# Kernel optimization log

Measured on AMD Instinct MI355X. Metric: run time of the kernel, lower is better.

## Reference

```python
import jax, jax.numpy as jnp
import numpy as np

H = 2048          # hidden_size
M = 512           # moe_intermediate_size
E = 8             # n_routed_experts
TOP_K = 2         # num_experts_per_tok
N_SHARED = 2      # n_shared_experts -> shared intermediate = M * N_SHARED
MS = M * N_SHARED
B, S = 2, 1024


def setup_inputs() -> dict:
    key = jax.random.key(0)
    ks = jax.random.split(key, 9)
    sc = 0.02
    return {
        "hidden_states": jax.random.normal(ks[0], (B, S, H), dtype=jnp.float32),
        "gate_w": jax.random.normal(ks[1], (E, H), dtype=jnp.float32) * sc,
        "Wg": jax.random.normal(ks[2], (E, H, M), dtype=jnp.float32) * sc,   # gate_proj per expert
        "Wu": jax.random.normal(ks[3], (E, H, M), dtype=jnp.float32) * sc,   # up_proj per expert
        "Wd": jax.random.normal(ks[4], (E, M, H), dtype=jnp.float32) * sc,   # down_proj per expert
        "sWg": jax.random.normal(ks[5], (H, MS), dtype=jnp.float32) * sc,    # shared gate_proj
        "sWu": jax.random.normal(ks[6], (H, MS), dtype=jnp.float32) * sc,    # shared up_proj
        "sWd": jax.random.normal(ks[7], (MS, H), dtype=jnp.float32) * sc,    # shared down_proj
    }


def reference(hidden_states, gate_w, Wg, Wu, Wd, sWg, sWu, sWd):
    b, s, h = hidden_states.shape
    x = hidden_states.reshape(-1, h)                     # [N, H]
    n = x.shape[0]

    # --- MoEGate: top-k routing with softmax over the selected logits ---
    logits = x @ gate_w.T                                # [N, E]
    topk_vals, topk_idx = jax.lax.top_k(logits, TOP_K)   # [N, K]
    w = jax.nn.softmax(topk_vals, axis=-1)               # softmax scoring over top-k
    # per-token combine weight for every expert (zero where not routed)
    comb = jnp.zeros((n, E), x.dtype).at[jnp.arange(n)[:, None], topk_idx].add(w)

    # --- Routed experts (SwiGLU MLP per expert); combine is the sparse
    #     weight matrix `comb`, mathematically identical to torch dispatch ---
    g = jnp.einsum('nh,ehm->enm', x, Wg)                 # [E, N, M]
    u = jnp.einsum('nh,ehm->enm', x, Wu)
    eo = jnp.einsum('enm,emh->enh', jax.nn.silu(g) * u, Wd)  # [E, N, H]
    y = jnp.einsum('ne,enh->nh', comb, eo)               # weighted combine

    # --- Shared experts (dense SwiGLU MLP on all tokens) ---
    y = y + (jax.nn.silu(x @ sWg) * (x @ sWu)) @ sWd
    return y.reshape(b, s, h)
```

## Files before the change

### kernel.cpp

```cpp
#include <hip/hip_runtime.h>

#define H 2048
#define MDIM 512
#define NE 8
#define MS 1024
#define NTOK 2048
#define ACT_R_ROWS 5120

typedef unsigned short u16;
typedef __attribute__((ext_vector_type(8))) short s16x8;
typedef __attribute__((ext_vector_type(4))) float f32x4;

__device__ inline u16 f2bf(float f) {
  unsigned u = __builtin_bit_cast(unsigned, f);
  u = (u + 0x7fffu + ((u >> 16) & 1u)) >> 16;
  return (u16)u;
}
__device__ inline float bf2f(u16 v) {
  return __builtin_bit_cast(float, (unsigned)v << 16);
}

__device__ inline f32x4 mfma16(s16x8 a, s16x8 b, f32x4 c) {
  return __builtin_amdgcn_mfma_f32_16x16x32_bf16(a, b, c, 0, 0, 0);
}

__device__ inline void gload16(const void* g, void* l) {
  __builtin_amdgcn_global_load_lds(
      (const __attribute__((address_space(1))) unsigned int*)g,
      (__attribute__((address_space(3))) unsigned int*)l, 16, 0, 0);
}


__global__ void k_cvt(const float* __restrict__ src, u16* __restrict__ dst, int n8) {
  int i = blockIdx.x * 256 + threadIdx.x;
  if (i >= n8) return;
  const f32x4* s = (const f32x4*)src;
  f32x4 a = s[2 * i + 0], b = s[2 * i + 1];
  s16x8 o;
  o[0] = (short)f2bf(a[0]); o[1] = (short)f2bf(a[1]);
  o[2] = (short)f2bf(a[2]); o[3] = (short)f2bf(a[3]);
  o[4] = (short)f2bf(b[0]); o[5] = (short)f2bf(b[1]);
  o[6] = (short)f2bf(b[2]); o[7] = (short)f2bf(b[3]);
  ((s16x8*)dst)[i] = o;
}

__device__ inline void tile_t64(const float* __restrict__ src, u16* __restrict__ dst,
                                int R, int C, int bx, int by) {
  __shared__ u16 tt[64][66];
  int c0 = bx * 64, r0 = by * 64;
  int t = threadIdx.x;
  int cq = (t & 15) * 4, rr = t >> 4;
  #pragma unroll
  for (int i = 0; i < 4; i++) {
    int row = rr + i * 16;
    f32x4 v = *(const f32x4*)&src[(long)(r0 + row) * C + c0 + cq];
    tt[cq + 0][row] = f2bf(v[0]);
    tt[cq + 1][row] = f2bf(v[1]);
    tt[cq + 2][row] = f2bf(v[2]);
    tt[cq + 3][row] = f2bf(v[3]);
  }
  __syncthreads();
  int c = t >> 2, ch = t & 3;
  #pragma unroll
  for (int h = 0; h < 2; h++) {
    int chunk = ch + h * 4;
    const u16* p = &tt[c][chunk * 8];
    s16x8 o;
    #pragma unroll
    for (int w0 = 0; w0 < 8; w0++) o[w0] = (short)p[w0];
    *(s16x8*)&dst[(long)(c0 + c) * R + r0 + chunk * 8] = o;
  }
}

__global__ __launch_bounds__(256) void k_prep(
    const float* __restrict__ Wg, const float* __restrict__ Wu,
    const float* __restrict__ Wd, const float* __restrict__ sWg,
    const float* __restrict__ sWu, const float* __restrict__ sWd,
    u16* __restrict__ WgT, u16* __restrict__ WuT, u16* __restrict__ WdT,
    u16* __restrict__ sWgT, u16* __restrict__ sWuT, u16* __restrict__ sWdT) {
  int b = blockIdx.x;
  const float* src; u16* dst; int R, C, lb;
  if (b < 2048) {
    lb = b; R = H; C = MDIM;
    int z = lb >> 8; lb &= 255;
    src = Wg + (size_t)z * H * MDIM; dst = WgT + (size_t)z * MDIM * H;
  } else if (b < 4096) {
    lb = b - 2048; R = H; C = MDIM;
    int z = lb >> 8; lb &= 255;
    src = Wu + (size_t)z * H * MDIM; dst = WuT + (size_t)z * MDIM * H;
  } else if (b < 6144) {
    lb = b - 4096; R = MDIM; C = H;
    int z = lb >> 8; lb &= 255;
    src = Wd + (size_t)z * MDIM * H; dst = WdT + (size_t)z * H * MDIM;
  } else if (b < 6656) {
    lb = b - 6144; R = H; C = MS; src = sWg; dst = sWgT;
  } else if (b < 7168) {
    lb = b - 6656; R = H; C = MS; src = sWu; dst = sWuT;
  } else {
    lb = b - 7168; R = MS; C = H; src = sWd; dst = sWdT;
  }
  int nbx = C >> 6;
  tile_t64(src, dst, R, C, lb % nbx, lb / nbx);
}


__global__ void k_logits(const float* __restrict__ x, const float* __restrict__ gw,
                         int* __restrict__ te, float* __restrict__ tw) {
  int n = blockIdx.x * 4 + (threadIdx.x >> 6);
  int lane = threadIdx.x & 63;
  double acc[NE];
  #pragma unroll
  for (int e = 0; e < NE; e++) acc[e] = 0.0;
  for (int j = lane; j < H; j += 64) {
    float xv = x[(long)n * H + j];
    #pragma unroll
    for (int e = 0; e < NE; e++) acc[e] += (double)xv * (double)gw[e * H + j];
  }
  #pragma unroll
  for (int off = 32; off; off >>= 1) {
    #pragma unroll
    for (int e = 0; e < NE; e++) acc[e] += __shfl_xor(acc[e], off);
  }
  if (lane == 0) {
    int b0 = 0; double v0 = acc[0];
    #pragma unroll
    for (int e = 1; e < NE; e++) { if (acc[e] > v0) { v0 = acc[e]; b0 = e; } }
    int b1 = -1; double v1 = -1e300;
    #pragma unroll
    for (int e = 0; e < NE; e++) { if (e != b0 && acc[e] > v1) { v1 = acc[e]; b1 = e; } }
    double ex = exp(v1 - v0);
    te[n * 2] = b0; te[n * 2 + 1] = b1;
    tw[n * 2] = (float)(1.0 / (1.0 + ex));
    tw[n * 2 + 1] = (float)(ex / (1.0 + ex));
  }
}

__global__ __launch_bounds__(256) void k_build(
    const int* __restrict__ te, const float* __restrict__ tw,
    int* __restrict__ counts, int* __restrict__ offs,
    int* __restrict__ perm, float* __restrict__ wgt, int* __restrict__ slotmap) {
  __shared__ int cnt[256][NE];
  __shared__ int pb[NE];
  int t = threadIdx.x;
  int ebuf[16];
  int lc[NE];
  #pragma unroll
  for (int e = 0; e < NE; e++) lc[e] = 0;
  #pragma unroll
  for (int i = 0; i < 16; i++) {
    int ei = te[t * 16 + i];
    ebuf[i] = ei;
    #pragma unroll
    for (int e = 0; e < NE; e++) lc[e] += (ei == e) ? 1 : 0;
  }
  #pragma unroll
  for (int e = 0; e < NE; e++) cnt[t][e] = lc[e];
  __syncthreads();
  if (t < NE) {
    int run = 0;
    for (int i = 0; i < 256; i++) { int v = cnt[i][t]; cnt[i][t] = run; run += v; }
    counts[t] = run;
  }
  __syncthreads();
  if (t == 0) {
    int off = 0;
    #pragma unroll
    for (int e = 0; e < NE; e++) {
      pb[e] = off; offs[e] = off;
      off += ((counts[e] + 127) >> 7) << 7;
    }
    offs[NE] = off;
  }
  for (int i = t; i < ACT_R_ROWS; i += 256) { perm[i] = 0; wgt[i] = 0.f; }
  __syncthreads();
  int run2[NE];
  #pragma unroll
  for (int e = 0; e < NE; e++) run2[e] = cnt[t][e];
  #pragma unroll
  for (int i = 0; i < 16; i++) {
    int ei = ebuf[i];
    int idx = 0;
    #pragma unroll
    for (int e = 0; e < NE; e++) {
      if (ei == e) idx = pb[e] + run2[e];
      run2[e] += (ei == e) ? 1 : 0;
    }
    perm[idx] = (t * 16 + i) >> 1;
    wgt[idx] = tw[t * 16 + i];
    slotmap[t * 16 + i] = idx;
  }
}

__global__ __launch_bounds__(256, 2) void k_gu(
    const u16* __restrict__ xbf, const u16* __restrict__ WgT, const u16* __restrict__ WuT,
    const u16* __restrict__ sWgT, const u16* __restrict__ sWuT,
    u16* __restrict__ act_s, u16* __restrict__ act_r,
    const int* __restrict__ perm, const int* __restrict__ counts,
    const int* __restrict__ offs) {
  int lin = blockIdx.x;
  int xcd = lin & 7, jj = lin >> 3;
  int g = xcd + 8 * (jj % 10);
  int bx = jj / 10;
  const u16 *Bg, *Bu;
  u16* act;
  int Nout, cnt, rowBase, by;
  bool gather;
  if (g < 16) {
    gather = false; by = g;
    cnt = NTOK; rowBase = bx * 128;
    Bg = sWgT + (size_t)by * 64 * H;
    Bu = sWuT + (size_t)by * 64 * H;
    act = act_s; Nout = MS;
  } else {
    gather = true;
    int e = (g - 16) >> 3; by = (g - 16) & 7;
    cnt = counts[e];
    if (bx * 128 >= cnt) return;
    rowBase = offs[e] + bx * 128;
    Bg = WgT + ((size_t)e * MDIM + (size_t)by * 64) * H;
    Bu = WuT + ((size_t)e * MDIM + (size_t)by * 64) * H;
    act = act_r; Nout = MDIM;
  }

  __shared__ char lds[2][32768];

  int tid = threadIdx.x;
  int wave = tid >> 6, lane = tid & 63;
  int wr = wave >> 1, wc = wave & 1;
  int la = lane & 15, ks = lane >> 4;

  int rIn = tid >> 3;
  int csrc = ((tid & 7) << 4) ^ ((rIn & 7) << 4);
  const char* srcA[4];
  const char* srcBg[2];
  const char* srcBu[2];
  #pragma unroll
  for (int j = 0; j < 4; j++) {
    int row = j * 32 + rIn;
    int tok = gather ? perm[rowBase + row] : (rowBase + row);
    srcA[j] = (const char*)xbf + (size_t)tok * H * 2 + csrc;
  }
  #pragma unroll
  for (int j = 0; j < 2; j++) {
    int row = j * 32 + rIn;
    srcBg[j] = (const char*)Bg + (size_t)row * H * 2 + csrc;
    srcBu[j] = (const char*)Bu + (size_t)row * H * 2 + csrc;
  }

  int offA[4][2], offB[2][2];
  #pragma unroll
  for (int m = 0; m < 4; m++) {
    int arow = wr * 64 + m * 16 + la;
    #pragma unroll
    for (int kk = 0; kk < 2; kk++) {
      int c = kk * 64 + ks * 16;
      offA[m][kk] = arow * 128 + (c ^ ((arow & 7) << 4));
    }
  }
  #pragma unroll
  for (int n = 0; n < 2; n++) {
    int brow = wc * 32 + n * 16 + la;
    #pragma unroll
    for (int kk = 0; kk < 2; kk++) {
      int c = kk * 64 + ks * 16;
      offB[n][kk] = brow * 128 + (c ^ ((brow & 7) << 4));
    }
  }

  f32x4 zero4 = {0.f, 0.f, 0.f, 0.f};
  f32x4 gacc[4][2], uacc[4][2];
  #pragma unroll
  for (int m = 0; m < 4; m++)
    #pragma unroll
    for (int n = 0; n < 2; n++) { gacc[m][n] = zero4; uacc[m][n] = zero4; }

  auto STAGE = [&](int p, int k0) {
    char* b = lds[p];
    #pragma unroll
    for (int j = 0; j < 4; j++)
      gload16(srcA[j] + k0, b + j * 4096 + wave * 1024);
    #pragma unroll
    for (int j = 0; j < 2; j++) {
      gload16(srcBg[j] + k0, b + 16384 + j * 4096 + wave * 1024);
      gload16(srcBu[j] + k0, b + 24576 + j * 4096 + wave * 1024);
    }
  };

  const int NT = H / 64;
  STAGE(0, 0);
  STAGE(1, 128);
  asm volatile("s_waitcnt vmcnt(8)" ::: "memory");
  __builtin_amdgcn_sched_barrier(0);
  __builtin_amdgcn_s_barrier();

  for (int t = 0; t < NT; ++t) {
    int p = t & 1;
    const char* A = lds[p];
    const char* G = lds[p] + 16384;
    const char* U = lds[p] + 24576;
    s16x8 af[2][4], gf[2][2], uf[2][2];
    #pragma unroll
    for (int kk = 0; kk < 2; kk++) {
      #pragma unroll
      for (int m = 0; m < 4; m++) af[kk][m] = *(const s16x8*)(A + offA[m][kk]);
      #pragma unroll
      for (int n = 0; n < 2; n++) {
        gf[kk][n] = *(const s16x8*)(G + offB[n][kk]);
        uf[kk][n] = *(const s16x8*)(U + offB[n][kk]);
      }
    }
    asm volatile("s_waitcnt lgkmcnt(0)" ::: "memory");
    __builtin_amdgcn_sched_barrier(0);
    __builtin_amdgcn_s_barrier();
    if (t + 2 < NT) STAGE(p, (t + 2) * 128);
    __builtin_amdgcn_sched_barrier(0);
    #pragma unroll
    for (int kk = 0; kk < 2; kk++) {
      #pragma unroll
      for (int m = 0; m < 4; m++) {
        #pragma unroll
        for (int n = 0; n < 2; n++) {
          gacc[m][n] = mfma16(af[kk][m], gf[kk][n], gacc[m][n]);
          uacc[m][n] = mfma16(af[kk][m], uf[kk][n], uacc[m][n]);
        }
      }
    }
    if (t + 2 < NT) { asm volatile("s_waitcnt vmcnt(8)" ::: "memory"); }
    else            { asm volatile("s_waitcnt vmcnt(0)" ::: "memory"); }
    __builtin_amdgcn_sched_barrier(0);
    __builtin_amdgcn_s_barrier();
  }

  #pragma unroll
  for (int m = 0; m < 4; m++) {
    #pragma unroll
    for (int n = 0; n < 2; n++) {
      #pragma unroll
      for (int r = 0; r < 4; r++) {
        int lr = wr * 64 + m * 16 + ks * 4 + r;
        int col = by * 64 + wc * 32 + n * 16 + la;
        float gg = gacc[m][n][r], uu = uacc[m][n][r];
        float a = gg / (1.0f + __expf(-gg)) * uu;
        if (gather && (bx * 128 + lr) >= cnt) a = 0.0f;
        act[(size_t)(rowBase + lr) * Nout + col] = f2bf(a);
      }
    }
  }
}

__global__ __launch_bounds__(256, 3) void k_down2(
    const u16* __restrict__ act_s, const u16* __restrict__ act_r,
    const u16* __restrict__ sWdT, const u16* __restrict__ WdT,
    float* __restrict__ y, u16* __restrict__ rdown,
    const float* __restrict__ wgt,
    const int* __restrict__ counts, const int* __restrict__ offs) {
  int lin = blockIdx.x;
  int xcd = lin & 7, jj = lin >> 3;
  int g = xcd + 8 * (jj % 36);
  int bx = jj / 36;
  const u16 *A, *B;
  int KD, NT, cnt, rowBase, by;
  bool routed;
  if (g < 32) {
    routed = false; by = g;
    KD = MS; NT = MS / 64;
    cnt = NTOK; rowBase = bx * 128;
    A = act_s + (size_t)rowBase * MS;
    B = sWdT + (size_t)by * 64 * MS;
  } else {
    routed = true;
    int e = (g - 32) >> 5; by = (g - 32) & 31;
    KD = MDIM; NT = MDIM / 64;
    cnt = counts[e];
    if (bx * 128 >= cnt) return;
    rowBase = offs[e] + bx * 128;
    A = act_r + (size_t)rowBase * MDIM;
    B = WdT + ((size_t)e * H + (size_t)by * 64) * MDIM;
  }

  __shared__ char lds[2][24576];

  int tid = threadIdx.x;
  int wave = tid >> 6, lane = tid & 63;
  int wr = wave >> 1, wc = wave & 1;
  int la = lane & 15, ks = lane >> 4;

  int rIn = tid >> 3;
  int csrc = ((tid & 7) << 4) ^ ((rIn & 7) << 4);
  const char* srcA[4];
  const char* srcB[2];
  #pragma unroll
  for (int j = 0; j < 4; j++) {
    int row = j * 32 + rIn;
    srcA[j] = (const char*)A + (size_t)row * KD * 2 + csrc;
  }
  #pragma unroll
  for (int j = 0; j < 2; j++) {
    int row = j * 32 + rIn;
    srcB[j] = (const char*)B + (size_t)row * KD * 2 + csrc;
  }

  int offA[4][2], offB[2][2];
  #pragma unroll
  for (int m = 0; m < 4; m++) {
    int arow = wr * 64 + m * 16 + la;
    #pragma unroll
    for (int kk = 0; kk < 2; kk++) {
      int c = kk * 64 + ks * 16;
      offA[m][kk] = arow * 128 + (c ^ ((arow & 7) << 4));
    }
  }
  #pragma unroll
  for (int n = 0; n < 2; n++) {
    int brow = wc * 32 + n * 16 + la;
    #pragma unroll
    for (int kk = 0; kk < 2; kk++) {
      int c = kk * 64 + ks * 16;
      offB[n][kk] = brow * 128 + (c ^ ((brow & 7) << 4));
    }
  }

  f32x4 zero4 = {0.f, 0.f, 0.f, 0.f};
  f32x4 acc[4][2];
  #pragma unroll
  for (int m = 0; m < 4; m++)
    #pragma unroll
    for (int n = 0; n < 2; n++) acc[m][n] = zero4;

  auto STAGE = [&](int p, int k0) {
    char* b = lds[p];
    #pragma unroll
    for (int j = 0; j < 4; j++)
      gload16(srcA[j] + k0, b + j * 4096 + wave * 1024);
    #pragma unroll
    for (int j = 0; j < 2; j++)
      gload16(srcB[j] + k0, b + 16384 + j * 4096 + wave * 1024);
  };

  STAGE(0, 0);
  STAGE(1, 128);
  asm volatile("s_waitcnt vmcnt(6)" ::: "memory");
  __builtin_amdgcn_sched_barrier(0);
  __builtin_amdgcn_s_barrier();

  for (int t = 0; t < NT; ++t) {
    int p = t & 1;
    const char* Ab = lds[p];
    const char* Bb = lds[p] + 16384;
    s16x8 af[2][4], bf[2][2];
    #pragma unroll
    for (int kk = 0; kk < 2; kk++) {
      #pragma unroll
      for (int m = 0; m < 4; m++) af[kk][m] = *(const s16x8*)(Ab + offA[m][kk]);
      #pragma unroll
      for (int n = 0; n < 2; n++) bf[kk][n] = *(const s16x8*)(Bb + offB[n][kk]);
    }
    asm volatile("s_waitcnt lgkmcnt(0)" ::: "memory");
    __builtin_amdgcn_sched_barrier(0);
    __builtin_amdgcn_s_barrier();
    if (t + 2 < NT) STAGE(p, (t + 2) * 128);
    __builtin_amdgcn_sched_barrier(0);
    #pragma unroll
    for (int kk = 0; kk < 2; kk++) {
      #pragma unroll
      for (int m = 0; m < 4; m++)
        #pragma unroll
        for (int n = 0; n < 2; n++) acc[m][n] = mfma16(af[kk][m], bf[kk][n], acc[m][n]);
    }
    if (t + 2 < NT) { asm volatile("s_waitcnt vmcnt(6)" ::: "memory"); }
    else            { asm volatile("s_waitcnt vmcnt(0)" ::: "memory"); }
    __builtin_amdgcn_sched_barrier(0);
    __builtin_amdgcn_s_barrier();
  }

  #pragma unroll
  for (int m = 0; m < 4; m++) {
    #pragma unroll
    for (int n = 0; n < 2; n++) {
      #pragma unroll
      for (int r = 0; r < 4; r++) {
        int lr = wr * 64 + m * 16 + ks * 4 + r;
        int col = by * 64 + wc * 32 + n * 16 + la;
        float v = acc[m][n][r];
        if (routed) {
          if (bx * 128 + lr < cnt) {
            int si = rowBase + lr;
            rdown[(size_t)si * H + col] = f2bf(wgt[si] * v);
          }
        } else {
          y[(size_t)(rowBase + lr) * H + col] = v;
        }
      }
    }
  }
}

__global__ __launch_bounds__(256) void k_combine(float* __restrict__ y,
                                                 const u16* __restrict__ rdown,
                                                 const int* __restrict__ slotmap) {
  int n = blockIdx.x;
  int s0 = slotmap[n * 2], s1 = slotmap[n * 2 + 1];
  const s16x8* r0 = (const s16x8*)(rdown + (size_t)s0 * H);
  const s16x8* r1 = (const s16x8*)(rdown + (size_t)s1 * H);
  f32x4* yp = (f32x4*)(y + (size_t)n * H);
  int t = threadIdx.x;
  s16x8 a = r0[t], b = r1[t];
  f32x4 y0 = yp[2 * t], y1 = yp[2 * t + 1];
  #pragma unroll
  for (int j = 0; j < 4; j++) {
    y0[j] += bf2f((u16)a[j]) + bf2f((u16)b[j]);
    y1[j] += bf2f((u16)a[4 + j]) + bf2f((u16)b[4 + j]);
  }
  yp[2 * t] = y0;
  yp[2 * t + 1] = y1;
}


extern "C" void kernel_launch(void* const* d_in, const int* in_sizes, int n_in,
                              void* d_out, int out_size, void* d_ws, size_t ws_size,
                              hipStream_t stream) {
  const float* x   = (const float*)d_in[0];
  const float* gw  = (const float*)d_in[1];
  const float* Wg  = (const float*)d_in[2];
  const float* Wu  = (const float*)d_in[3];
  const float* Wd  = (const float*)d_in[4];
  const float* sWg = (const float*)d_in[5];
  const float* sWu = (const float*)d_in[6];
  const float* sWd = (const float*)d_in[7];
  float* y = (float*)d_out;

  char* w = (char*)d_ws;
  auto alloc = [&](size_t bytes) {
    char* p = w;
    w += (bytes + 255) & ~(size_t)255;
    return p;
  };
  u16* xbf   = (u16*)alloc((size_t)NTOK * H * 2);
  u16* WgT   = (u16*)alloc((size_t)NE * MDIM * H * 2);
  u16* WuT   = (u16*)alloc((size_t)NE * MDIM * H * 2);
  u16* WdT   = (u16*)alloc((size_t)NE * H * MDIM * 2);
  u16* sWgT  = (u16*)alloc((size_t)MS * H * 2);
  u16* sWuT  = (u16*)alloc((size_t)MS * H * 2);
  u16* sWdT  = (u16*)alloc((size_t)H * MS * 2);
  u16* act_s = (u16*)alloc((size_t)NTOK * MS * 2);
  u16* act_r = (u16*)alloc((size_t)ACT_R_ROWS * MDIM * 2);
  u16* rdown = (u16*)alloc((size_t)ACT_R_ROWS * H * 2);
  int*   te      = (int*)alloc((size_t)NTOK * 2 * 4);
  float* tw      = (float*)alloc((size_t)NTOK * 2 * 4);
  int*   counts  = (int*)alloc(64);
  int*   offs    = (int*)alloc(64);
  int*   perm    = (int*)alloc((size_t)ACT_R_ROWS * 4);
  float* wgt     = (float*)alloc((size_t)ACT_R_ROWS * 4);
  int*   slotmap = (int*)alloc((size_t)NTOK * 2 * 4);

  k_logits<<<NTOK / 4, 256, 0, stream>>>(x, gw, te, tw);
  k_build<<<1, 256, 0, stream>>>(te, tw, counts, offs, perm, wgt, slotmap);

  int n8 = NTOK * H / 8;
  k_cvt<<<(n8 + 255) / 256, 256, 0, stream>>>(x, xbf, n8);
  k_prep<<<7680, 256, 0, stream>>>(Wg, Wu, Wd, sWg, sWu, sWd,
                                   WgT, WuT, WdT, sWgT, sWuT, sWdT);

  k_gu<<<80 * 16, 256, 0, stream>>>(
      xbf, WgT, WuT, sWgT, sWuT, act_s, act_r, perm, counts, offs);

  k_down2<<<288 * 16, 256, 0, stream>>>(
      act_s, act_r, sWdT, WdT, y, rdown, wgt, counts, offs);

  k_combine<<<NTOK, 256, 0, stream>>>(y, rdown, slotmap);
}
```

Baseline: 168.6 us.

## Widen GEMM N-tiles to 128 and fuse x bf16 conversion into router logits

Both grouped GEMM kernels (gate/up and down) now use 128x128 output tiles instead of 128x64. Each wave computes a 4x4 MFMA fragment grid, and the LDS fragment loads are split into two k-halves with a partial lgkmcnt wait. This raises arithmetic intensity per staged tile and halves the number of blocks, at the cost of more LDS per block and more accumulator registers, with occupancy bounds lowered to 1 and 2. Separately, the fp32-to-bf16 conversion of x is folded into the router logits kernel, which now reads x with vectorized loads, removing one launch and one extra pass over x.

```diff
diff --git a/kernel.cpp b/kernel.cpp
--- a/kernel.cpp
+++ b/kernel.cpp
@@ -8,6 +8,7 @@
 #define ACT_R_ROWS 5120
 
 typedef unsigned short u16;
+typedef __attribute__((ext_vector_type(4))) short s16x4;
 typedef __attribute__((ext_vector_type(8))) short s16x8;
 typedef __attribute__((ext_vector_type(4))) float f32x4;
 
@@ -31,18 +32,107 @@
 }
 
 
-__global__ void k_cvt(const float* __restrict__ src, u16* __restrict__ dst, int n8) {
-  int i = blockIdx.x * 256 + threadIdx.x;
-  if (i >= n8) return;
-  const f32x4* s = (const f32x4*)src;
-  f32x4 a = s[2 * i + 0], b = s[2 * i + 1];
-  s16x8 o;
-  o[0] = (short)f2bf(a[0]); o[1] = (short)f2bf(a[1]);
-  o[2] = (short)f2bf(a[2]); o[3] = (short)f2bf(a[3]);
-  o[4] = (short)f2bf(b[0]); o[5] = (short)f2bf(b[1]);
-  o[6] = (short)f2bf(b[2]); o[7] = (short)f2bf(b[3]);
-  ((s16x8*)dst)[i] = o;
-}
+__global__ __launch_bounds__(256) void k_xlog(const float* __restrict__ x,
+                                              const float* __restrict__ gw,
+                                              u16* __restrict__ xbf,
+                                              int* __restrict__ te, float* __restrict__ tw) {
+  int n = blockIdx.x * 4 + (threadIdx.x >> 6);
+  int lane = threadIdx.x & 63;
+  double acc[NE];
+  #pragma unroll
+  for (int e = 0; e < NE; e++) acc[e] = 0.0;
+  const f32x4* xr = (const f32x4*)(x + (size_t)n * H);
+  s16x4* xo = (s16x4*)(xbf + (size_t)n * H);
+  #pragma unroll
+  for (int it = 0; it < H / 256; it++) {
+    int j4 = it * 64 + lane;
+    f32x4 v = xr[j4];
+    s16x4 o;
+    o[0] = (short)f2bf(v[0]); o[1] = (short)f2bf(v[1]);
+    o[2] = (short)f2bf(v[2]); o[3] = (short)f2bf(v[3]);
+    xo[j4] = o;
+    #pragma unroll
+    for (int e = 0; e < NE; e++) {
+      f32x4 g = *(const f32x4*)&gw[e * H + j4 * 4];
+      acc[e] += (double)v[0] * g[0] + (double)v[1] * g[1] +
+                (double)v[2] * g[2] + (double)v[3] * g[3];
+    }
+  }
+  #pragma unroll
+  for (int off = 32; off; off >>= 1) {
+    #pragma unroll
+    for (int e = 0; e < NE; e++) acc[e] += __shfl_xor(acc[e], off);
+  }
+  if (lane == 0) {
+    int b0 = 0; double v0 = acc[0];
+    #pragma unroll
+    for (int e = 1; e < NE; e++) { if (acc[e] > v0) { v0 = acc[e]; b0 = e; } }
+    int b1 = -1; double v1 = -1e300;
+    #pragma unroll
+    for (int e = 0; e < NE; e++) { if (e != b0 && acc[e] > v1) { v1 = acc[e]; b1 = e; } }
+    double ex = exp(v1 - v0);
+    te[n * 2] = b0; te[n * 2 + 1] = b1;
+    tw[n * 2] = (float)(1.0 / (1.0 + ex));
+    tw[n * 2 + 1] = (float)(ex / (1.0 + ex));
+  }
+}
+
+__global__ __launch_bounds__(256) void k_build(
+    const int* __restrict__ te, const float* __restrict__ tw,
+    int* __restrict__ counts, int* __restrict__ offs,
+    int* __restrict__ perm, float* __restrict__ wgt, int* __restrict__ slotmap) {
+  __shared__ int cnt[256][NE];
+  __shared__ int pb[NE];
+  int t = threadIdx.x;
+  int ebuf[16];
+  int lc[NE];
+  #pragma unroll
+  for (int e = 0; e < NE; e++) lc[e] = 0;
+  #pragma unroll
+  for (int i = 0; i < 16; i++) {
+    int ei = te[t * 16 + i];
+    ebuf[i] = ei;
+    #pragma unroll
+    for (int e = 0; e < NE; e++) lc[e] += (ei == e) ? 1 : 0;
+  }
+  #pragma unroll
+  for (int e = 0; e < NE; e++) cnt[t][e] = lc[e];
+  __syncthreads();
+  if (t < NE) {
+    int run = 0;
+    for (int i = 0; i < 256; i++) { int v = cnt[i][t]; cnt[i][t] = run; run += v; }
+    counts[t] = run;
+  }
+  __syncthreads();
+  if (t == 0) {
+    int off = 0;
+    #pragma unroll
+    for (int e = 0; e < NE; e++) {
+      pb[e] = off; offs[e] = off;
+      off += ((counts[e] + 127) >> 7) << 7;
+    }
+    offs[NE] = off;
+  }
+  for (int i = t; i < ACT_R_ROWS; i += 256) { perm[i] = 0; wgt[i] = 0.f; }
+  __syncthreads();
+  int run2[NE];
+  #pragma unroll
+  for (int e = 0; e < NE; e++) run2[e] = cnt[t][e];
+  #pragma unroll
+  for (int i = 0; i < 16; i++) {
+    int ei = ebuf[i];
+    int idx = 0;
+    #pragma unroll
+    for (int e = 0; e < NE; e++) {
+      if (ei == e) idx = pb[e] + run2[e];
+      run2[e] += (ei == e) ? 1 : 0;
+    }
+    perm[idx] = (t * 16 + i) >> 1;
+    wgt[idx] = tw[t * 16 + i];
+    slotmap[t * 16 + i] = idx;
+  }
+}
+
 
 __device__ inline void tile_t64(const float* __restrict__ src, u16* __restrict__ dst,
                                 int R, int C, int bx, int by) {
@@ -103,95 +193,7 @@
   tile_t64(src, dst, R, C, lb % nbx, lb / nbx);
 }
 
-
-__global__ void k_logits(const float* __restrict__ x, const float* __restrict__ gw,
-                         int* __restrict__ te, float* __restrict__ tw) {
-  int n = blockIdx.x * 4 + (threadIdx.x >> 6);
-  int lane = threadIdx.x & 63;
-  double acc[NE];
-  #pragma unroll
-  for (int e = 0; e < NE; e++) acc[e] = 0.0;
-  for (int j = lane; j < H; j += 64) {
-    float xv = x[(long)n * H + j];
-    #pragma unroll
-    for (int e = 0; e < NE; e++) acc[e] += (double)xv * (double)gw[e * H + j];
-  }
-  #pragma unroll
-  for (int off = 32; off; off >>= 1) {
-    #pragma unroll
-    for (int e = 0; e < NE; e++) acc[e] += __shfl_xor(acc[e], off);
-  }
-  if (lane == 0) {
-    int b0 = 0; double v0 = acc[0];
-    #pragma unroll
-    for (int e = 1; e < NE; e++) { if (acc[e] > v0) { v0 = acc[e]; b0 = e; } }
-    int b1 = -1; double v1 = -1e300;
-    #pragma unroll
-    for (int e = 0; e < NE; e++) { if (e != b0 && acc[e] > v1) { v1 = acc[e]; b1 = e; } }
-    double ex = exp(v1 - v0);
-    te[n * 2] = b0; te[n * 2 + 1] = b1;
-    tw[n * 2] = (float)(1.0 / (1.0 + ex));
-    tw[n * 2 + 1] = (float)(ex / (1.0 + ex));
-  }
-}
-
-__global__ __launch_bounds__(256) void k_build(
-    const int* __restrict__ te, const float* __restrict__ tw,
-    int* __restrict__ counts, int* __restrict__ offs,
-    int* __restrict__ perm, float* __restrict__ wgt, int* __restrict__ slotmap) {
-  __shared__ int cnt[256][NE];
-  __shared__ int pb[NE];
-  int t = threadIdx.x;
-  int ebuf[16];
-  int lc[NE];
-  #pragma unroll
-  for (int e = 0; e < NE; e++) lc[e] = 0;
-  #pragma unroll
-  for (int i = 0; i < 16; i++) {
-    int ei = te[t * 16 + i];
-    ebuf[i] = ei;
-    #pragma unroll
-    for (int e = 0; e < NE; e++) lc[e] += (ei == e) ? 1 : 0;
-  }
-  #pragma unroll
-  for (int e = 0; e < NE; e++) cnt[t][e] = lc[e];
-  __syncthreads();
-  if (t < NE) {
-    int run = 0;
-    for (int i = 0; i < 256; i++) { int v = cnt[i][t]; cnt[i][t] = run; run += v; }
-    counts[t] = run;
-  }
-  __syncthreads();
-  if (t == 0) {
-    int off = 0;
-    #pragma unroll
-    for (int e = 0; e < NE; e++) {
-      pb[e] = off; offs[e] = off;
-      off += ((counts[e] + 127) >> 7) << 7;
-    }
-    offs[NE] = off;
-  }
-  for (int i = t; i < ACT_R_ROWS; i += 256) { perm[i] = 0; wgt[i] = 0.f; }
-  __syncthreads();
-  int run2[NE];
-  #pragma unroll
-  for (int e = 0; e < NE; e++) run2[e] = cnt[t][e];
-  #pragma unroll
-  for (int i = 0; i < 16; i++) {
-    int ei = ebuf[i];
-    int idx = 0;
-    #pragma unroll
-    for (int e = 0; e < NE; e++) {
-      if (ei == e) idx = pb[e] + run2[e];
-      run2[e] += (ei == e) ? 1 : 0;
-    }
-    perm[idx] = (t * 16 + i) >> 1;
-    wgt[idx] = tw[t * 16 + i];
-    slotmap[t * 16 + i] = idx;
-  }
-}
-
-__global__ __launch_bounds__(256, 2) void k_gu(
+__global__ __launch_bounds__(256, 1) void k_gu(
     const u16* __restrict__ xbf, const u16* __restrict__ WgT, const u16* __restrict__ WuT,
     const u16* __restrict__ sWgT, const u16* __restrict__ sWuT,
     u16* __restrict__ act_s, u16* __restrict__ act_r,
@@ -199,30 +201,30 @@
     const int* __restrict__ offs) {
   int lin = blockIdx.x;
   int xcd = lin & 7, jj = lin >> 3;
-  int g = xcd + 8 * (jj % 10);
-  int bx = jj / 10;
+  int g = xcd + 8 * (jj % 5);
+  int bx = jj / 5;
   const u16 *Bg, *Bu;
   u16* act;
   int Nout, cnt, rowBase, by;
   bool gather;
-  if (g < 16) {
+  if (g < 8) {
     gather = false; by = g;
     cnt = NTOK; rowBase = bx * 128;
-    Bg = sWgT + (size_t)by * 64 * H;
-    Bu = sWuT + (size_t)by * 64 * H;
+    Bg = sWgT + (size_t)by * 128 * H;
+    Bu = sWuT + (size_t)by * 128 * H;
     act = act_s; Nout = MS;
   } else {
     gather = true;
-    int e = (g - 16) >> 3; by = (g - 16) & 7;
+    int e = (g - 8) >> 2; by = (g - 8) & 3;
     cnt = counts[e];
     if (bx * 128 >= cnt) return;
     rowBase = offs[e] + bx * 128;
-    Bg = WgT + ((size_t)e * MDIM + (size_t)by * 64) * H;
-    Bu = WuT + ((size_t)e * MDIM + (size_t)by * 64) * H;
+    Bg = WgT + ((size_t)e * MDIM + (size_t)by * 128) * H;
+    Bu = WuT + ((size_t)e * MDIM + (size_t)by * 128) * H;
     act = act_r; Nout = MDIM;
   }
 
-  __shared__ char lds[2][32768];
+  __shared__ char lds[2][49152];
 
   int tid = threadIdx.x;
   int wave = tid >> 6, lane = tid & 63;
@@ -231,48 +233,35 @@
 
   int rIn = tid >> 3;
   int csrc = ((tid & 7) << 4) ^ ((rIn & 7) << 4);
-  const char* srcA[4];
-  const char* srcBg[2];
-  const char* srcBu[2];
+  const char *srcA[4], *srcBg[4], *srcBu[4];
   #pragma unroll
   for (int j = 0; j < 4; j++) {
     int row = j * 32 + rIn;
     int tok = gather ? perm[rowBase + row] : (rowBase + row);
-    srcA[j] = (const char*)xbf + (size_t)tok * H * 2 + csrc;
-  }
-  #pragma unroll
-  for (int j = 0; j < 2; j++) {
-    int row = j * 32 + rIn;
+    srcA[j]  = (const char*)xbf + (size_t)tok * H * 2 + csrc;
     srcBg[j] = (const char*)Bg + (size_t)row * H * 2 + csrc;
     srcBu[j] = (const char*)Bu + (size_t)row * H * 2 + csrc;
   }
 
-  int offA[4][2], offB[2][2];
+  int offA[4][2], offB[4][2];
   #pragma unroll
   for (int m = 0; m < 4; m++) {
     int arow = wr * 64 + m * 16 + la;
+    int brow = wc * 64 + m * 16 + la;
     #pragma unroll
     for (int kk = 0; kk < 2; kk++) {
       int c = kk * 64 + ks * 16;
       offA[m][kk] = arow * 128 + (c ^ ((arow & 7) << 4));
-    }
-  }
-  #pragma unroll
-  for (int n = 0; n < 2; n++) {
-    int brow = wc * 32 + n * 16 + la;
-    #pragma unroll
-    for (int kk = 0; kk < 2; kk++) {
-      int c = kk * 64 + ks * 16;
-      offB[n][kk] = brow * 128 + (c ^ ((brow & 7) << 4));
+      offB[m][kk] = brow * 128 + (c ^ ((brow & 7) << 4));
     }
   }
 
   f32x4 zero4 = {0.f, 0.f, 0.f, 0.f};
-  f32x4 gacc[4][2], uacc[4][2];
+  f32x4 gacc[4][4], uacc[4][4];
   #pragma unroll
   for (int m = 0; m < 4; m++)
     #pragma unroll
-    for (int n = 0; n < 2; n++) { gacc[m][n] = zero4; uacc[m][n] = zero4; }
+    for (int n = 0; n < 4; n++) { gacc[m][n] = zero4; uacc[m][n] = zero4; }
 
   auto STAGE = [&](int p, int k0) {
     char* b = lds[p];
@@ -280,16 +269,17 @@
     for (int j = 0; j < 4; j++)
       gload16(srcA[j] + k0, b + j * 4096 + wave * 1024);
     #pragma unroll
-    for (int j = 0; j < 2; j++) {
+    for (int j = 0; j < 4; j++)
       gload16(srcBg[j] + k0, b + 16384 + j * 4096 + wave * 1024);
-      gload16(srcBu[j] + k0, b + 24576 + j * 4096 + wave * 1024);
-    }
+    #pragma unroll
+    for (int j = 0; j < 4; j++)
+      gload16(srcBu[j] + k0, b + 32768 + j * 4096 + wave * 1024);
   };
 
   const int NT = H / 64;
   STAGE(0, 0);
   STAGE(1, 128);
-  asm volatile("s_waitcnt vmcnt(8)" ::: "memory");
+  asm volatile("s_waitcnt vmcnt(12)" ::: "memory");
   __builtin_amdgcn_sched_barrier(0);
   __builtin_amdgcn_s_barrier();
 
@@ -297,16 +287,26 @@
     int p = t & 1;
     const char* A = lds[p];
     const char* G = lds[p] + 16384;
-    const char* U = lds[p] + 24576;
-    s16x8 af[2][4], gf[2][2], uf[2][2];
-    #pragma unroll
-    for (int kk = 0; kk < 2; kk++) {
+    const char* U = lds[p] + 32768;
+    s16x8 a0[4], g0[4], u0[4], a1[4], g1[4], u1[4];
+    #pragma unroll
+    for (int m = 0; m < 4; m++) a0[m] = *(const s16x8*)(A + offA[m][0]);
+    #pragma unroll
+    for (int n = 0; n < 4; n++) { g0[n] = *(const s16x8*)(G + offB[n][0]);
+                                  u0[n] = *(const s16x8*)(U + offB[n][0]); }
+    #pragma unroll
+    for (int m = 0; m < 4; m++) a1[m] = *(const s16x8*)(A + offA[m][1]);
+    #pragma unroll
+    for (int n = 0; n < 4; n++) { g1[n] = *(const s16x8*)(G + offB[n][1]);
+                                  u1[n] = *(const s16x8*)(U + offB[n][1]); }
+    asm volatile("s_waitcnt lgkmcnt(12)" ::: "memory");
+    __builtin_amdgcn_sched_barrier(0);
+    #pragma unroll
+    for (int m = 0; m < 4; m++) {
       #pragma unroll
-      for (int m = 0; m < 4; m++) af[kk][m] = *(const s16x8*)(A + offA[m][kk]);
-      #pragma unroll
-      for (int n = 0; n < 2; n++) {
-        gf[kk][n] = *(const s16x8*)(G + offB[n][kk]);
-        uf[kk][n] = *(const s16x8*)(U + offB[n][kk]);
+      for (int n = 0; n < 4; n++) {
+        gacc[m][n] = mfma16(a0[m], g0[n], gacc[m][n]);
+        uacc[m][n] = mfma16(a0[m], u0[n], uacc[m][n]);
       }
     }
     asm volatile("s_waitcnt lgkmcnt(0)" ::: "memory");
@@ -315,17 +315,14 @@
     if (t + 2 < NT) STAGE(p, (t + 2) * 128);
     __builtin_amdgcn_sched_barrier(0);
     #pragma unroll
-    for (int kk = 0; kk < 2; kk++) {
+    for (int m = 0; m < 4; m++) {
       #pragma unroll
-      for (int m = 0; m < 4; m++) {
-        #pragma unroll
-        for (int n = 0; n < 2; n++) {
-          gacc[m][n] = mfma16(af[kk][m], gf[kk][n], gacc[m][n]);
-          uacc[m][n] = mfma16(af[kk][m], uf[kk][n], uacc[m][n]);
-        }
+      for (int n = 0; n < 4; n++) {
+        gacc[m][n] = mfma16(a1[m], g1[n], gacc[m][n]);
+        uacc[m][n] = mfma16(a1[m], u1[n], uacc[m][n]);
       }
     }
-    if (t + 2 < NT) { asm volatile("s_waitcnt vmcnt(8)" ::: "memory"); }
+    if (t + 2 < NT) { asm volatile("s_waitcnt vmcnt(12)" ::: "memory"); }
     else            { asm volatile("s_waitcnt vmcnt(0)" ::: "memory"); }
     __builtin_amdgcn_sched_barrier(0);
     __builtin_amdgcn_s_barrier();
@@ -334,11 +331,11 @@
   #pragma unroll
   for (int m = 0; m < 4; m++) {
     #pragma unroll
-    for (int n = 0; n < 2; n++) {
+    for (int n = 0; n < 4; n++) {
       #pragma unroll
       for (int r = 0; r < 4; r++) {
         int lr = wr * 64 + m * 16 + ks * 4 + r;
-        int col = by * 64 + wc * 32 + n * 16 + la;
+        int col = by * 128 + wc * 64 + n * 16 + la;
         float gg = gacc[m][n][r], uu = uacc[m][n][r];
         float a = gg / (1.0f + __expf(-gg)) * uu;
         if (gather && (bx * 128 + lr) >= cnt) a = 0.0f;
@@ -348,7 +345,7 @@
   }
 }
 
-__global__ __launch_bounds__(256, 3) void k_down2(
+__global__ __launch_bounds__(256, 2) void k_down2(
     const u16* __restrict__ act_s, const u16* __restrict__ act_r,
     const u16* __restrict__ sWdT, const u16* __restrict__ WdT,
     float* __restrict__ y, u16* __restrict__ rdown,
@@ -356,29 +353,29 @@
     const int* __restrict__ counts, const int* __restrict__ offs) {
   int lin = blockIdx.x;
   int xcd = lin & 7, jj = lin >> 3;
-  int g = xcd + 8 * (jj % 36);
-  int bx = jj / 36;
+  int g = xcd + 8 * (jj % 18);
+  int bx = jj / 18;
   const u16 *A, *B;
   int KD, NT, cnt, rowBase, by;
   bool routed;
-  if (g < 32) {
+  if (g < 16) {
     routed = false; by = g;
     KD = MS; NT = MS / 64;
     cnt = NTOK; rowBase = bx * 128;
     A = act_s + (size_t)rowBase * MS;
-    B = sWdT + (size_t)by * 64 * MS;
+    B = sWdT + (size_t)by * 128 * MS;
   } else {
     routed = true;
-    int e = (g - 32) >> 5; by = (g - 32) & 31;
+    int e = (g - 16) >> 4; by = (g - 16) & 15;
     KD = MDIM; NT = MDIM / 64;
     cnt = counts[e];
     if (bx * 128 >= cnt) return;
     rowBase = offs[e] + bx * 128;
     A = act_r + (size_t)rowBase * MDIM;
-    B = WdT + ((size_t)e * H + (size_t)by * 64) * MDIM;
-  }
-
-  __shared__ char lds[2][24576];
+    B = WdT + ((size_t)e * H + (size_t)by * 128) * MDIM;
+  }
+
+  __shared__ char lds[2][32768];
 
   int tid = threadIdx.x;
   int wave = tid >> 6, lane = tid & 63;
@@ -387,45 +384,33 @@
 
   int rIn = tid >> 3;
   int csrc = ((tid & 7) << 4) ^ ((rIn & 7) << 4);
-  const char* srcA[4];
-  const char* srcB[2];
+  const char *srcA[4], *srcB[4];
   #pragma unroll
   for (int j = 0; j < 4; j++) {
     int row = j * 32 + rIn;
     srcA[j] = (const char*)A + (size_t)row * KD * 2 + csrc;
-  }
-  #pragma unroll
-  for (int j = 0; j < 2; j++) {
-    int row = j * 32 + rIn;
     srcB[j] = (const char*)B + (size_t)row * KD * 2 + csrc;
   }
 
-  int offA[4][2], offB[2][2];
+  int offA[4][2], offB[4][2];
   #pragma unroll
   for (int m = 0; m < 4; m++) {
     int arow = wr * 64 + m * 16 + la;
+    int brow = wc * 64 + m * 16 + la;
     #pragma unroll
     for (int kk = 0; kk < 2; kk++) {
       int c = kk * 64 + ks * 16;
       offA[m][kk] = arow * 128 + (c ^ ((arow & 7) << 4));
-    }
-  }
-  #pragma unroll
-  for (int n = 0; n < 2; n++) {
-    int brow = wc * 32 + n * 16 + la;
-    #pragma unroll
-    for (int kk = 0; kk < 2; kk++) {
-      int c = kk * 64 + ks * 16;
-      offB[n][kk] = brow * 128 + (c ^ ((brow & 7) << 4));
+      offB[m][kk] = brow * 128 + (c ^ ((brow & 7) << 4));
     }
   }
 
   f32x4 zero4 = {0.f, 0.f, 0.f, 0.f};
-  f32x4 acc[4][2];
+  f32x4 acc[4][4];
   #pragma unroll
   for (int m = 0; m < 4; m++)
     #pragma unroll
-    for (int n = 0; n < 2; n++) acc[m][n] = zero4;
+    for (int n = 0; n < 4; n++) acc[m][n] = zero4;
 
   auto STAGE = [&](int p, int k0) {
     char* b = lds[p];
@@ -433,13 +418,13 @@
     for (int j = 0; j < 4; j++)
       gload16(srcA[j] + k0, b + j * 4096 + wave * 1024);
     #pragma unroll
-    for (int j = 0; j < 2; j++)
+    for (int j = 0; j < 4; j++)
       gload16(srcB[j] + k0, b + 16384 + j * 4096 + wave * 1024);
   };
 
   STAGE(0, 0);
   STAGE(1, 128);
-  asm volatile("s_waitcnt vmcnt(6)" ::: "memory");
+  asm volatile("s_waitcnt vmcnt(8)" ::: "memory");
   __builtin_amdgcn_sched_barrier(0);
   __builtin_amdgcn_s_barrier();
 
@@ -447,48 +432,56 @@
     int p = t & 1;
     const char* Ab = lds[p];
     const char* Bb = lds[p] + 16384;
-    s16x8 af[2][4], bf[2][2];
-    #pragma unroll
-    for (int kk = 0; kk < 2; kk++) {
+    s16x8 a0[4], b0[4], a1[4], b1[4];
+    #pragma unroll
+    for (int m = 0; m < 4; m++) a0[m] = *(const s16x8*)(Ab + offA[m][0]);
+    #pragma unroll
+    for (int n = 0; n < 4; n++) b0[n] = *(const s16x8*)(Bb + offB[n][0]);
+    #pragma unroll
+    for (int m = 0; m < 4; m++) a1[m] = *(const s16x8*)(Ab + offA[m][1]);
+    #pragma unroll
+    for (int n = 0; n < 4; n++) b1[n] = *(const s16x8*)(Bb + offB[n][1]);
+    asm volatile("s_waitcnt lgkmcnt(8)" ::: "memory");
+    __builtin_amdgcn_sched_barrier(0);
+    #pragma unroll
+    for (int m = 0; m < 4; m++)
       #pragma unroll
-      for (int m = 0; m < 4; m++) af[kk][m] = *(const s16x8*)(Ab + offA[m][kk]);
-      #pragma unroll
-      for (int n = 0; n < 2; n++) bf[kk][n] = *(const s16x8*)(Bb + offB[n][kk]);
-    }
+      for (int n = 0; n < 4; n++) acc[m][n] = mfma16(a0[m], b0[n], acc[m][n]);
     asm volatile("s_waitcnt lgkmcnt(0)" ::: "memory");
     __builtin_amdgcn_sched_barrier(0);
     __builtin_amdgcn_s_barrier();
     if (t + 2 < NT) STAGE(p, (t + 2) * 128);
     __builtin_amdgcn_sched_barrier(0);
     #pragma unroll
-    for (int kk = 0; kk < 2; kk++) {
+    for (int m = 0; m < 4; m++)
       #pragma unroll
-      for (int m = 0; m < 4; m++)
+      for (int n = 0; n < 4; n++) acc[m][n] = mfma16(a1[m], b1[n], acc[m][n]);
+    if (t + 2 < NT) { asm volatile("s_waitcnt vmcnt(8)" ::: "memory"); }
+    else            { asm volatile("s_waitcnt vmcnt(0)" ::: "memory"); }
+    __builtin_amdgcn_sched_barrier(0);
+    __builtin_amdgcn_s_barrier();
+  }
+
+  #pragma unroll
+  for (int m = 0; m < 4; m++) {
+    #pragma unroll
+    for (int r = 0; r < 4; r++) {
+      int lr = wr * 64 + m * 16 + ks * 4 + r;
+      if (routed) {
+        if (bx * 128 + lr < cnt) {
+          int si = rowBase + lr;
+          float wv = wgt[si];
+          #pragma unroll
+          for (int n = 0; n < 4; n++) {
+            int col = by * 128 + wc * 64 + n * 16 + la;
+            rdown[(size_t)si * H + col] = f2bf(wv * acc[m][n][r]);
+          }
+        }
+      } else {
         #pragma unroll
-        for (int n = 0; n < 2; n++) acc[m][n] = mfma16(af[kk][m], bf[kk][n], acc[m][n]);
-    }
-    if (t + 2 < NT) { asm volatile("s_waitcnt vmcnt(6)" ::: "memory"); }
-    else            { asm volatile("s_waitcnt vmcnt(0)" ::: "memory"); }
-    __builtin_amdgcn_sched_barrier(0);
-    __builtin_amdgcn_s_barrier();
-  }
-
-  #pragma unroll
-  for (int m = 0; m < 4; m++) {
-    #pragma unroll
-    for (int n = 0; n < 2; n++) {
-      #pragma unroll
-      for (int r = 0; r < 4; r++) {
-        int lr = wr * 64 + m * 16 + ks * 4 + r;
-        int col = by * 64 + wc * 32 + n * 16 + la;
-        float v = acc[m][n][r];
-        if (routed) {
-          if (bx * 128 + lr < cnt) {
-            int si = rowBase + lr;
-            rdown[(size_t)si * H + col] = f2bf(wgt[si] * v);
-          }
-        } else {
-          y[(size_t)(rowBase + lr) * H + col] = v;
+        for (int n = 0; n < 4; n++) {
+          int col = by * 128 + wc * 64 + n * 16 + la;
+          y[(size_t)(rowBase + lr) * H + col] = acc[m][n][r];
         }
       }
     }
@@ -553,18 +546,16 @@
   float* wgt     = (float*)alloc((size_t)ACT_R_ROWS * 4);
   int*   slotmap = (int*)alloc((size_t)NTOK * 2 * 4);
 
-  k_logits<<<NTOK / 4, 256, 0, stream>>>(x, gw, te, tw);
+  k_xlog<<<NTOK / 4, 256, 0, stream>>>(x, gw, xbf, te, tw);
   k_build<<<1, 256, 0, stream>>>(te, tw, counts, offs, perm, wgt, slotmap);
 
-  int n8 = NTOK * H / 8;
-  k_cvt<<<(n8 + 255) / 256, 256, 0, stream>>>(x, xbf, n8);
   k_prep<<<7680, 256, 0, stream>>>(Wg, Wu, Wd, sWg, sWu, sWd,
                                    WgT, WuT, WdT, sWgT, sWuT, sWdT);
 
-  k_gu<<<80 * 16, 256, 0, stream>>>(
+  k_gu<<<8 * 5 * 16, 256, 0, stream>>>(
       xbf, WgT, WuT, sWgT, sWuT, act_s, act_r, perm, counts, offs);
 
-  k_down2<<<288 * 16, 256, 0, stream>>>(
+  k_down2<<<8 * 18 * 16, 256, 0, stream>>>(
       act_s, act_r, sWdT, WdT, y, rdown, wgt, counts, offs);
 
   k_combine<<<NTOK, 256, 0, stream>>>(y, rdown, slotmap);
```

Result: slower. 191.6 us (+13.6%).
